# Optimization experiments

Hardware: AMD Instinct MI355X
Metric: run time of the kernel (lower is better)

Reference implementation:

```python
import jax, jax.numpy as jnp
import numpy as np

V = 100000
NNZ = 1600000
B = 4
C_IN = 64
C_HID = 128
C_OUT = 64
K = 4
BN_EPS = 1e-5


def cheb_conv(x, rows, cols, vals, W, b):
    # x: (B, Cin, V); W: (K, Cin, Cout); b: (Cout,)
    Bn, Cin, Vn = x.shape
    Kn = W.shape[0]

    def spmm(y):  # y: (V, F) -> L @ y via edge-list scatter-add
        return jax.ops.segment_sum(vals[:, None] * y[cols], rows, num_segments=Vn)

    x0 = jnp.transpose(x, (2, 0, 1)).reshape(Vn, Bn * Cin)  # (V, B*Cin)
    xs = [x0]
    if Kn > 1:
        x1 = spmm(x0)
        xs.append(x1)
        for _ in range(2, Kn):
            x2 = 2.0 * spmm(x1) - x0  # Chebyshev recurrence
            xs.append(x2)
            x0, x1 = x1, x2
    Xk = jnp.stack(xs, 0).reshape(Kn, Vn, Bn, Cin)  # (K, V, B, Cin)
    out = jnp.einsum('kvbi,kio->bov', Xk, W)  # (B, Cout, V)
    return out + b[None, :, None]


def batch_norm(x, gamma, beta):
    # BatchNorm1d on (B, C, V): stats over (B, V), biased variance (training mode)
    mean = jnp.mean(x, axis=(0, 2), keepdims=True)
    var = jnp.mean(jnp.square(x - mean), axis=(0, 2), keepdims=True)
    xn = (x - mean) * jax.lax.rsqrt(var + BN_EPS)
    return xn * gamma[None, :, None] + beta[None, :, None]


def setup_inputs() -> dict:
    key = jax.random.key(0)
    ks = jax.random.split(key, 8)
    x = jax.random.normal(ks[0], (B, C_IN, V), dtype=jnp.float32)
    lap_rows = jax.random.randint(ks[1], (NNZ,), 0, V, dtype=jnp.int32)
    lap_cols = jax.random.randint(ks[2], (NNZ,), 0, V, dtype=jnp.int32)
    # scale so the effective Laplacian spectral norm is ~O(1) (Chebyshev assumes rescaled L)
    lap_vals = jax.random.normal(ks[3], (NNZ,), dtype=jnp.float32) * 0.01
    w1 = jax.random.normal(ks[4], (K, C_IN, C_HID), dtype=jnp.float32) * (1.0 / np.sqrt(K * C_IN))
    b1 = jnp.zeros((C_HID,), dtype=jnp.float32)
    bn_gamma = jnp.ones((C_HID,), dtype=jnp.float32)
    bn_beta = jnp.zeros((C_HID,), dtype=jnp.float32)
    w2 = jax.random.normal(ks[5], (K, C_HID, C_OUT), dtype=jnp.float32) * (1.0 / np.sqrt(K * C_HID))
    b2 = jnp.zeros((C_OUT,), dtype=jnp.float32)
    return {"x": x, "lap_rows": lap_rows, "lap_cols": lap_cols, "lap_vals": lap_vals,
            "w1": w1, "b1": b1, "bn_gamma": bn_gamma, "bn_beta": bn_beta,
            "w2": w2, "b2": b2}


def reference(x, lap_rows, lap_cols, lap_vals, w1, b1, bn_gamma, bn_beta, w2, b2):
    out = cheb_conv(x, lap_rows, lap_cols, lap_vals, w1, b1)
    out = jax.nn.relu(out)
    out = batch_norm(out, bn_gamma, bn_beta)
    out = cheb_conv(out, lap_rows, lap_cols, lap_vals, w2, b2)
    # in_channels == out_channels -> resizer is Identity
    return jax.nn.relu(out + x)
```

## Files before the change

kernel.cpp:

```cpp
#include <hip/hip_runtime.h>

#define V 100000
#define NNZ 1600000
#define RSLOT 64

typedef unsigned short ushort_t;
typedef unsigned int uint_t;
typedef unsigned long long ull_t;
typedef __attribute__((ext_vector_type(4))) float f32x4;
typedef __attribute__((ext_vector_type(8))) short bf16x8;

__device__ __forceinline__ float bf2f(ushort_t u) {
    union { uint_t i; float f; } x; x.i = ((uint_t)u) << 16; return x.f;
}
__device__ __forceinline__ ushort_t f2bf(float f) {
    union { float f; uint_t i; } x; x.f = f;
    uint_t u = x.i;
    return (ushort_t)((u + 0x7fffu + ((u >> 16) & 1u)) >> 16);
}
__device__ __forceinline__ float blo(uint_t u) {
    union { uint_t i; float f; } x; x.i = u << 16; return x.f;
}
__device__ __forceinline__ float bhi(uint_t u) {
    union { uint_t i; float f; } x; x.i = u & 0xffff0000u; return x.f;
}
__device__ __forceinline__ uint_t pk(float a, float b) {
    return (uint_t)f2bf(a) | ((uint_t)f2bf(b) << 16);
}
__device__ __forceinline__ void unpack8(uint4 u, float* f) {
    f[0] = blo(u.x); f[1] = bhi(u.x); f[2] = blo(u.y); f[3] = bhi(u.y);
    f[4] = blo(u.z); f[5] = bhi(u.z); f[6] = blo(u.w); f[7] = bhi(u.w);
}
__device__ __forceinline__ uint4 pack8(const float* f) {
    uint4 u;
    u.x = pk(f[0], f[1]); u.y = pk(f[2], f[3]);
    u.z = pk(f[4], f[5]); u.w = pk(f[6], f[7]);
    return u;
}

__global__ void diag_k(float* __restrict__ out, float code) {
    if (threadIdx.x == 0 && blockIdx.x == 0) out[0] = code;
}

__global__ __launch_bounds__(256) void pack_x0_k(const float* __restrict__ x,
                                                 ushort_t* __restrict__ x0) {
    __shared__ float tile[32][33];
    int v0 = blockIdx.x * 32, j0 = blockIdx.y * 32;
    int tx = threadIdx.x & 31, ty = threadIdx.x >> 5;
    for (int jj = ty; jj < 32; jj += 8)
        tile[jj][tx] = x[(size_t)(j0 + jj) * V + v0 + tx];
    __syncthreads();
    for (int vv = ty; vv < 32; vv += 8)
        x0[(size_t)(v0 + vv) * 256 + j0 + tx] = f2bf(tile[tx][vv]);
}

__global__ __launch_bounds__(256) void prep_w_k(const float* __restrict__ w1,
                                                const float* __restrict__ w2,
                                                ushort_t* __restrict__ wp1,
                                                ushort_t* __restrict__ wp2) {
    int idx = blockIdx.x * 256 + threadIdx.x;
    if (idx < 32768) {
        int f = idx;
        int j = f & 7, ch = (f >> 3) & 127, q = (f >> 10) & 3, kb = (f >> 12) & 3, L = (f >> 14) & 1;
        int k = kb * 32 + q * 8 + j;
        int t = L * 2 + (k >> 6), i = k & 63;
        wp1[idx] = f2bf(w1[((size_t)t * 64 + i) * 128 + ch]);
    } else {
        int f = idx - 32768;
        int j = f & 7, o = (f >> 3) & 63, q = (f >> 9) & 3, kb = (f >> 11) & 3, t = (f >> 13) & 3;
        int k = kb * 32 + q * 8 + j;
        wp2[f] = f2bf(w2[((size_t)t * 128 + k) * 64 + o]);
    }
}

__global__ __launch_bounds__(256) void scatter_k(const int* __restrict__ rows,
                                                 const int* __restrict__ cols,
                                                 const float* __restrict__ vals,
                                                 int* __restrict__ cnt,
                                                 int2* __restrict__ edges) {
    int e = blockIdx.x * 256 + threadIdx.x;
    int r = rows[e];
    int pos = atomicAdd(&cnt[r], 1);
    edges[r * RSLOT + pos] = make_int2(cols[e], __float_as_int(vals[e]));
}

__global__ __launch_bounds__(256) void spmm_wave(const int* __restrict__ cnt,
                                                 const int2* __restrict__ edges,
                                                 const ushort_t* __restrict__ y,
                                                 const ushort_t* __restrict__ z,
                                                 float alpha, float beta,
                                                 ushort_t* __restrict__ out) {
    int v = __builtin_amdgcn_readfirstlane((blockIdx.x * 256 + threadIdx.x) >> 6);
    if (v >= V) return;
    int l = threadIdx.x & 63;
    const ushort_t* yl = y + l * 4;

    float a0 = 0.f, a1 = 0.f, a2 = 0.f, a3 = 0.f;
    int e0 = v * RSLOT;
    int e1 = e0 + __builtin_amdgcn_readfirstlane(cnt[v]);
    int e = e0;
    for (; e + 8 <= e1; e += 8) {
        int2 ed[8];
#pragma unroll
        for (int i = 0; i < 8; ++i) ed[i] = edges[e + i];
        uint2 u[8];
#pragma unroll
        for (int i = 0; i < 8; ++i) u[i] = *(const uint2*)(yl + (size_t)ed[i].x * 256);
#pragma unroll
        for (int i = 0; i < 8; ++i) {
            float wv = __int_as_float(ed[i].y);
            a0 += wv * blo(u[i].x);
            a1 += wv * bhi(u[i].x);
            a2 += wv * blo(u[i].y);
            a3 += wv * bhi(u[i].y);
        }
    }
    auto masked4 = [&](int base, int c4) {
        int2 ed[4];
#pragma unroll
        for (int i = 0; i < 4; ++i) ed[i] = edges[i < c4 ? base + i : e0];
        uint2 u[4];
#pragma unroll
        for (int i = 0; i < 4; ++i) u[i] = *(const uint2*)(yl + (size_t)ed[i].x * 256);
#pragma unroll
        for (int i = 0; i < 4; ++i) {
            float wv = (i < c4) ? __int_as_float(ed[i].y) : 0.f;
            a0 += wv * blo(u[i].x);
            a1 += wv * bhi(u[i].x);
            a2 += wv * blo(u[i].y);
            a3 += wv * bhi(u[i].y);
        }
    };
    int rem = e1 - e;
    if (rem > 0) masked4(e, rem > 4 ? 4 : rem);
    if (rem > 4) masked4(e + 4, rem - 4);

    float r0 = alpha * a0, r1 = alpha * a1, r2 = alpha * a2, r3 = alpha * a3;
    if (z) {
        ull_t zt = __builtin_nontemporal_load(
            (const ull_t*)(z + (size_t)v * 256 + l * 4));
        r0 += beta * blo((uint_t)zt);
        r1 += beta * bhi((uint_t)zt);
        r2 += beta * blo((uint_t)(zt >> 32));
        r3 += beta * bhi((uint_t)(zt >> 32));
    }
    uint2 st;
    st.x = (uint_t)f2bf(r0) | ((uint_t)f2bf(r1) << 16);
    st.y = (uint_t)f2bf(r2) | ((uint_t)f2bf(r3) << 16);
    *(uint2*)(out + (size_t)v * 256 + l * 4) = st;
}

__global__ __launch_bounds__(256) void gemm1_mfma(const ushort_t* __restrict__ t0,
                                                  const ushort_t* __restrict__ t1,
                                                  const ushort_t* __restrict__ wp,
                                                  const float* __restrict__ b1,
                                                  ushort_t* __restrict__ rb,
                                                  int first, int last) {
    __shared__ uint4 s_buf[1088];
    uint4* s_a = s_buf;
    float* smem = (float*)s_buf;
    int tid = threadIdx.x;
    int l = tid & 63, w = tid >> 6;
    int q = l >> 4, n16 = l & 15;
    int b = blockIdx.y;
    int v0 = blockIdx.x * 64;

    {
        int row = tid >> 3, c = tid & 7;
        int row2 = row + 32;
        int va = v0 + row;  va = va < V ? va : V - 1;
        int vb = v0 + row2; vb = vb < V ? vb : V - 1;
        size_t ga = (size_t)va * 256 + b * 64 + c * 8;
        size_t gb = (size_t)vb * 256 + b * 64 + c * 8;
        s_a[row * 8 + (c ^ (row & 7))] = *(const uint4*)(t0 + ga);
        s_a[row2 * 8 + (c ^ (row2 & 7))] = *(const uint4*)(t0 + gb);
        s_a[512 + row * 8 + (c ^ (row & 7))] = *(const uint4*)(t1 + ga);
        s_a[512 + row2 * 8 + (c ^ (row2 & 7))] = *(const uint4*)(t1 + gb);
    }
    __syncthreads();

    f32x4 acc[8];
#pragma unroll
    for (int ct = 0; ct < 8; ++ct) acc[ct] = (f32x4){0.f, 0.f, 0.f, 0.f};

    int arow = w * 16 + n16;
#pragma unroll
    for (int kb = 0; kb < 4; ++kb) {
        int T = kb >> 1;
        bf16x8 a = *(const bf16x8*)&s_a[T * 512 + arow * 8 + (((kb & 1) * 4 + q) ^ (arow & 7))];
#pragma unroll
        for (int ct = 0; ct < 8; ++ct) {
            bf16x8 bf = *(const bf16x8*)(wp + (size_t)(((kb * 4 + q) * 128) + ct * 16 + n16) * 8);
            acc[ct] = __builtin_amdgcn_mfma_f32_16x16x32_bf16(a, bf, acc[ct], 0, 0, 0);
        }
    }
    __syncthreads();

    int row_d = tid >> 3;
    int c8 = tid & 7;
#pragma unroll
    for (int h = 0; h < 2; ++h) {
        if (h) __syncthreads();
#pragma unroll
        for (int ct = 0; ct < 4; ++ct)
#pragma unroll
            for (int r = 0; r < 4; ++r)
                smem[(w * 16 + q * 4 + r) * 66 + ct * 16 + n16] = acc[h * 4 + ct][r];
        __syncthreads();

        int ch0 = h * 64 + c8 * 8;
        float bc[8];
        if (last) {
#pragma unroll
            for (int j = 0; j < 8; ++j) bc[j] = b1[ch0 + j];
        }
#pragma unroll
        for (int k = 0; k < 2; ++k) {
            int row = row_d + k * 32;
            int v = v0 + row;
            bool valid = v < V;
            float vals[8];
#pragma unroll
            for (int j = 0; j < 8; ++j) vals[j] = smem[row * 66 + c8 * 8 + j];
            ushort_t* p = rb + (size_t)(valid ? v : 0) * 512 + b * 128 + ch0;
            if (!first && valid) {
                uint4 old = *(const uint4*)p;
                float of[8];
                unpack8(old, of);
#pragma unroll
                for (int j = 0; j < 8; ++j) vals[j] += of[j];
            }
            if (last) {
#pragma unroll
                for (int j = 0; j < 8; ++j) vals[j] = fmaxf(vals[j] + bc[j], 0.f);
            }
            if (valid) *(uint4*)p = pack8(vals);
        }
    }
}

__global__ __launch_bounds__(256) void stats_k(const ushort_t* __restrict__ rb,
                                               float* __restrict__ stats) {
    __shared__ float s_sum[128], s_sq[128];
    int tid = threadIdx.x;
    if (tid < 128) { s_sum[tid] = 0.f; s_sq[tid] = 0.f; }
    __syncthreads();
    int g = tid & 15, t16 = tid >> 4;
    float cs[8], cq[8];
#pragma unroll
    for (int j = 0; j < 8; ++j) { cs[j] = 0.f; cq[j] = 0.f; }
    for (int idx = blockIdx.x * 16 + t16; idx < V * 4; idx += 256 * 16) {
        int v = idx >> 2, bb = idx & 3;
        uint4 u = *(const uint4*)(rb + (size_t)v * 512 + bb * 128 + g * 8);
        float f[8];
        unpack8(u, f);
#pragma unroll
        for (int j = 0; j < 8; ++j) { cs[j] += f[j]; cq[j] += f[j] * f[j]; }
    }
#pragma unroll
    for (int j = 0; j < 8; ++j) {
        cs[j] += __shfl_xor(cs[j], 16); cs[j] += __shfl_xor(cs[j], 32);
        cq[j] += __shfl_xor(cq[j], 16); cq[j] += __shfl_xor(cq[j], 32);
    }
    if ((tid & 63) < 16) {
#pragma unroll
        for (int j = 0; j < 8; ++j) {
            atomicAdd(&s_sum[g * 8 + j], cs[j]);
            atomicAdd(&s_sq[g * 8 + j], cq[j]);
        }
    }
    __syncthreads();
    if (tid < 128) {
        atomicAdd(&stats[tid], s_sum[tid]);
        atomicAdd(&stats[128 + tid], s_sq[tid]);
    }
}

__global__ void finalize_k(const float* __restrict__ stats,
                           const float* __restrict__ gamma,
                           const float* __restrict__ beta,
                           float* __restrict__ ss) {
    int c = threadIdx.x;
    float n = (float)(4 * V);
    float mean = stats[c] / n;
    float var = stats[128 + c] / n - mean * mean;
    float inv = rsqrtf(var + 1e-5f);
    float sc = gamma[c] * inv;
    ss[c] = sc;
    ss[128 + c] = beta[c] - mean * sc;
}

__global__ __launch_bounds__(256) void gemmC_mfma(const ushort_t* __restrict__ rb,
                                                  const ushort_t* __restrict__ wp,
                                                  const ushort_t* S,
                                                  const float* __restrict__ ss,
                                                  ushort_t* P) {
    __shared__ float s_ss[256];
    __shared__ uint4 s_buf[1088];
    uint4* s_rb = s_buf;
    float* smem = (float*)s_buf;
    int tid = threadIdx.x;
    s_ss[tid] = ss[tid];
    int l = tid & 63, w = tid >> 6;
    int q = l >> 4, n16 = l & 15;
    int b = blockIdx.y;
    int v0 = blockIdx.x * 64;

#pragma unroll
    for (int k = 0; k < 4; ++k) {
        int idx = tid + k * 256;
        int row = idx >> 4, c = idx & 15;
        int v = v0 + row; v = v < V ? v : V - 1;
        s_rb[row * 16 + (c ^ (row & 7))] = *(const uint4*)(rb + (size_t)v * 512 + b * 128 + c * 8);
    }
    __syncthreads();

    f32x4 acc[4];
#pragma unroll
    for (int ct = 0; ct < 4; ++ct) acc[ct] = (f32x4){0.f, 0.f, 0.f, 0.f};

    int arow = w * 16 + n16;
#pragma unroll
    for (int kb = 0; kb < 4; ++kb) {
        int chl = kb * 32 + q * 8;
        bf16x8 a = *(const bf16x8*)&s_rb[arow * 16 + ((kb * 4 + q) ^ (arow & 7))];
#pragma unroll
        for (int j = 0; j < 8; ++j) {
            float f = bf2f((ushort_t)a[j]) * s_ss[chl + j] + s_ss[128 + chl + j];
            a[j] = (short)f2bf(f);
        }
#pragma unroll
        for (int ct = 0; ct < 4; ++ct) {
            bf16x8 bf = *(const bf16x8*)(wp + (size_t)(((kb * 4 + q) * 64) + ct * 16 + n16) * 8);
            acc[ct] = __builtin_amdgcn_mfma_f32_16x16x32_bf16(a, bf, acc[ct], 0, 0, 0);
        }
    }
    __syncthreads();

#pragma unroll
    for (int ct = 0; ct < 4; ++ct)
#pragma unroll
        for (int r = 0; r < 4; ++r)
            smem[(w * 16 + q * 4 + r) * 66 + ct * 16 + n16] = acc[ct][r];
    __syncthreads();

#pragma unroll
    for (int k = 0; k < 2; ++k) {
        int seg = tid + k * 256;
        int row = seg >> 3;
        int o0 = (seg & 7) * 8;
        int v = v0 + row;
        if (v >= V) continue;
        float vals[8];
#pragma unroll
        for (int j = 0; j < 8; ++j) vals[j] = smem[row * 66 + o0 + j];
        size_t idx = (size_t)v * 256 + b * 64 + o0;
        if (S) {
            uint4 sv = *(const uint4*)(S + idx);
            float sf[8];
            unpack8(sv, sf);
#pragma unroll
            for (int j = 0; j < 8; ++j) vals[j] += sf[j];
        }
        *(uint4*)(P + idx) = pack8(vals);
    }
}

__global__ __launch_bounds__(256) void gemm2_final(const ushort_t* __restrict__ rb,
                                                   const ushort_t* __restrict__ wp,
                                                   const ushort_t* __restrict__ Tb,
                                                   const float* __restrict__ b2,
                                                   const float* __restrict__ xres,
                                                   const float* __restrict__ ss,
                                                   float* __restrict__ out) {
    __shared__ float s_ss[256];
    __shared__ float s_b2[64];
    __shared__ uint_t s_tb[64 * 36];
    __shared__ uint4 s_rb[1024];
    int tid = threadIdx.x;
    s_ss[tid] = ss[tid];
    if (tid < 64) s_b2[tid] = b2[tid];
    int l = tid & 63, w = tid >> 6;
    int q = l >> 4, n16 = l & 15;
    int b = blockIdx.y;
    int v0 = blockIdx.x * 64;

#pragma unroll
    for (int k = 0; k < 2; ++k) {
        int seg = tid + k * 256;
        int row = seg >> 3, c = seg & 7;
        uint4 t = make_uint4(0u, 0u, 0u, 0u);
        if (v0 + row < V) t = *(const uint4*)(Tb + (size_t)(v0 + row) * 256 + b * 64 + c * 8);
        *(uint4*)&s_tb[row * 36 + c * 4] = t;
    }
#pragma unroll
    for (int k = 0; k < 4; ++k) {
        int idx = tid + k * 256;
        int row = idx >> 4, c = idx & 15;
        int v = v0 + row; v = v < V ? v : V - 1;
        s_rb[row * 16 + (c ^ (row & 7))] = *(const uint4*)(rb + (size_t)v * 512 + b * 128 + c * 8);
    }
    __syncthreads();

    f32x4 acc[4];
#pragma unroll
    for (int rt = 0; rt < 4; ++rt) acc[rt] = (f32x4){0.f, 0.f, 0.f, 0.f};

    int vl = w * 16 + n16;
#pragma unroll
    for (int kb = 0; kb < 4; ++kb) {
        int chl = kb * 32 + q * 8;
        bf16x8 t = *(const bf16x8*)&s_rb[vl * 16 + ((kb * 4 + q) ^ (vl & 7))];
#pragma unroll
        for (int j = 0; j < 8; ++j) {
            float f = bf2f((ushort_t)t[j]) * s_ss[chl + j] + s_ss[128 + chl + j];
            t[j] = (short)f2bf(f);
        }
#pragma unroll
        for (int rt = 0; rt < 4; ++rt) {
            bf16x8 af = *(const bf16x8*)(wp + (size_t)(((kb * 4 + q) * 64) + rt * 16 + n16) * 8);
            acc[rt] = __builtin_amdgcn_mfma_f32_16x16x32_bf16(af, t, acc[rt], 0, 0, 0);
        }
    }

    int v = v0 + vl;
    bool valid = v < V;
    int vv = valid ? v : 0;
#pragma unroll
    for (int rt = 0; rt < 4; ++rt)
#pragma unroll
        for (int r = 0; r < 4; ++r) {
            int o = rt * 16 + q * 4 + r;
            uint_t pr = s_tb[vl * 36 + rt * 8 + q * 2 + (r >> 1)];
            float tb = (r & 1) ? bhi(pr) : blo(pr);
            size_t idx = (size_t)(b * 64 + o) * V + vv;
            float val = acc[rt][r] + tb + s_b2[o] + xres[idx];
            if (valid) out[idx] = fmaxf(val, 0.f);
        }
}

extern "C" void kernel_launch(void* const* d_in, const int* in_sizes, int n_in,
                              void* d_out, int out_size, void* d_ws, size_t ws_size,
                              hipStream_t stream) {
    const float* x = (const float*)d_in[0];
    const int* lap_rows = (const int*)d_in[1];
    const int* lap_cols = (const int*)d_in[2];
    const float* lap_vals = (const float*)d_in[3];
    const float* w1 = (const float*)d_in[4];
    const float* b1 = (const float*)d_in[5];
    const float* bn_gamma = (const float*)d_in[6];
    const float* bn_beta = (const float*)d_in[7];
    const float* w2 = (const float*)d_in[8];
    const float* b2 = (const float*)d_in[9];
    float* out = (float*)d_out;

    char* ws = (char*)d_ws;
    size_t off = 0;
    auto alloc = [&](size_t bytes) {
        size_t r = off;
        off = (off + bytes + 255) & ~(size_t)255;
        return r;
    };
    size_t reg1_off = alloc((size_t)V * 512 * 2);
    size_t rb_off   = alloc((size_t)V * 512 * 2);
    size_t ed_off   = alloc((size_t)V * RSLOT * 8);
    size_t cur_off  = alloc((size_t)V * 4);
    size_t st_off   = alloc(256 * 4);
    size_t ss_off   = alloc(256 * 4);
    size_t wp1_off  = alloc(32768 * 2);
    size_t wp2_off  = alloc(32768 * 2);

    if (ws_size < off) {
        diag_k<<<1, 64, 0, stream>>>(out, 1000.f + (float)(ws_size >> 20));
        return;
    }

    ushort_t* slotA = (ushort_t*)(ws + reg1_off);
    ushort_t* slotB = slotA + (size_t)V * 256;
    ushort_t* rb = (ushort_t*)(ws + rb_off);
    int2* edges = (int2*)(ws + ed_off);
    int* cnt = (int*)(ws + cur_off);
    float* stats = (float*)(ws + st_off);
    float* ss = (float*)(ws + ss_off);
    ushort_t* wp1 = (ushort_t*)(ws + wp1_off);
    ushort_t* wp2 = (ushort_t*)(ws + wp2_off);

    const int SG = (V + 3) / 4;
    const ushort_t* nullu = (const ushort_t*)nullptr;

    hipMemsetAsync(cnt, 0, (size_t)V * 4, stream);
    hipMemsetAsync(stats, 0, 256 * 4, stream);

    pack_x0_k<<<dim3(V / 32, 8), 256, 0, stream>>>(x, slotA);
    prep_w_k<<<256, 256, 0, stream>>>(w1, w2, wp1, wp2);
    scatter_k<<<NNZ / 256, 256, 0, stream>>>(lap_rows, lap_cols, lap_vals, cnt, edges);

    dim3 g1((V + 63) / 64, 4);

    spmm_wave<<<SG, 256, 0, stream>>>(cnt, edges, slotA, nullu, 1.f, 0.f, slotB);
    gemm1_mfma<<<g1, 256, 0, stream>>>(slotA, slotB, wp1, b1, rb, 1, 0);
    spmm_wave<<<SG, 256, 0, stream>>>(cnt, edges, slotB, slotA, 2.f, -1.f, slotA);
    spmm_wave<<<SG, 256, 0, stream>>>(cnt, edges, slotA, slotB, 2.f, -1.f, slotB);
    gemm1_mfma<<<g1, 256, 0, stream>>>(slotA, slotB, wp1 + 16384, b1, rb, 0, 1);

    stats_k<<<256, 256, 0, stream>>>(rb, stats);
    finalize_k<<<1, 128, 0, stream>>>(stats, bn_gamma, bn_beta, ss);

    gemmC_mfma<<<g1, 256, 0, stream>>>(rb, wp2 + 3 * 8192, nullu, ss, slotA);
    spmm_wave<<<SG, 256, 0, stream>>>(cnt, edges, slotA, nullu, 2.f, 0.f, slotB);
    gemmC_mfma<<<g1, 256, 0, stream>>>(rb, wp2 + 2 * 8192, slotB, ss, slotB);
    spmm_wave<<<SG, 256, 0, stream>>>(cnt, edges, slotB, slotA, 2.f, -1.f, slotA);
    gemmC_mfma<<<g1, 256, 0, stream>>>(rb, wp2 + 1 * 8192, slotA, ss, slotA);
    spmm_wave<<<SG, 256, 0, stream>>>(cnt, edges, slotA, slotB, 1.f, -1.f, slotB);
    gemm2_final<<<g1, 256, 0, stream>>>(rb, wp2, slotB, b2, x, ss, out);
}
```

Before: 1.330 ms.

## Fuse BN statistics into layer-1 GEMM and merge K=4 GEMM passes

Folds the batch-norm sum and sum-of-squares reduction into the epilogue of the first-layer GEMM, so the separate stats kernel no longer re-reads the hidden activation buffer. When workspace allows, it also keeps all four Chebyshev terms in separate buffers and runs a single GEMM over K=256. This avoids the read-modify-write of the partial result and saves one launch. The cost is a larger workspace, which falls back to the old two-pass GEMM path if unavailable, plus extra shuffles and atomics in the epilogue.

New measurement: 1.410 ms. +6.0%, slower.

```diff
diff --git a/kernel.cpp b/kernel.cpp
--- a/kernel.cpp
+++ b/kernel.cpp
@@ -155,8 +155,10 @@
                                                   const ushort_t* __restrict__ wp,
                                                   const float* __restrict__ b1,
                                                   ushort_t* __restrict__ rb,
+                                                  float* __restrict__ stats,
                                                   int first, int last) {
     __shared__ uint4 s_buf[1088];
+    __shared__ float s_sum[128], s_sq[128];
     uint4* s_a = s_buf;
     float* smem = (float*)s_buf;
     int tid = threadIdx.x;
@@ -164,6 +166,7 @@
     int q = l >> 4, n16 = l & 15;
     int b = blockIdx.y;
     int v0 = blockIdx.x * 64;
+    if (tid < 128) { s_sum[tid] = 0.f; s_sq[tid] = 0.f; }
 
     {
         int row = tid >> 3, c = tid & 7;
@@ -214,6 +217,9 @@
 #pragma unroll
             for (int j = 0; j < 8; ++j) bc[j] = b1[ch0 + j];
         }
+        float csum[8], csq[8];
+#pragma unroll
+        for (int j = 0; j < 8; ++j) { csum[j] = 0.f; csq[j] = 0.f; }
 #pragma unroll
         for (int k = 0; k < 2; ++k) {
             int row = row_d + k * 32;
@@ -233,40 +239,145 @@
             if (last) {
 #pragma unroll
                 for (int j = 0; j < 8; ++j) vals[j] = fmaxf(vals[j] + bc[j], 0.f);
+                if (valid) {
+#pragma unroll
+                    for (int j = 0; j < 8; ++j) { csum[j] += vals[j]; csq[j] += vals[j] * vals[j]; }
+                }
             }
             if (valid) *(uint4*)p = pack8(vals);
         }
-    }
-}
-
-__global__ __launch_bounds__(256) void stats_k(const ushort_t* __restrict__ rb,
-                                               float* __restrict__ stats) {
+        if (last) {
+#pragma unroll
+            for (int j = 0; j < 8; ++j) {
+                csum[j] += __shfl_xor(csum[j], 8);
+                csum[j] += __shfl_xor(csum[j], 16);
+                csum[j] += __shfl_xor(csum[j], 32);
+                csq[j] += __shfl_xor(csq[j], 8);
+                csq[j] += __shfl_xor(csq[j], 16);
+                csq[j] += __shfl_xor(csq[j], 32);
+            }
+            if (l == c8) {
+#pragma unroll
+                for (int j = 0; j < 8; ++j) {
+                    atomicAdd(&s_sum[ch0 + j], csum[j]);
+                    atomicAdd(&s_sq[ch0 + j], csq[j]);
+                }
+            }
+        }
+    }
+    if (last) {
+        __syncthreads();
+        if (tid < 128) {
+            atomicAdd(&stats[tid], s_sum[tid]);
+            atomicAdd(&stats[128 + tid], s_sq[tid]);
+        }
+    }
+}
+
+__global__ __launch_bounds__(256) void gemm1K256(const ushort_t* __restrict__ x0b,
+                                                 const ushort_t* __restrict__ x1b,
+                                                 const ushort_t* __restrict__ x2b,
+                                                 const ushort_t* __restrict__ x3b,
+                                                 const ushort_t* __restrict__ wp,
+                                                 const float* __restrict__ b1,
+                                                 ushort_t* __restrict__ rb,
+                                                 float* __restrict__ stats) {
+    __shared__ uint4 s_buf[1088];
     __shared__ float s_sum[128], s_sq[128];
+    uint4* s_a = s_buf;
+    float* smem = (float*)s_buf;
     int tid = threadIdx.x;
+    int l = tid & 63, w = tid >> 6;
+    int q = l >> 4, n16 = l & 15;
+    int b = blockIdx.y;
+    int v0 = blockIdx.x * 64;
     if (tid < 128) { s_sum[tid] = 0.f; s_sq[tid] = 0.f; }
-    __syncthreads();
-    int g = tid & 15, t16 = tid >> 4;
-    float cs[8], cq[8];
-#pragma unroll
-    for (int j = 0; j < 8; ++j) { cs[j] = 0.f; cq[j] = 0.f; }
-    for (int idx = blockIdx.x * 16 + t16; idx < V * 4; idx += 256 * 16) {
-        int v = idx >> 2, bb = idx & 3;
-        uint4 u = *(const uint4*)(rb + (size_t)v * 512 + bb * 128 + g * 8);
-        float f[8];
-        unpack8(u, f);
-#pragma unroll
-        for (int j = 0; j < 8; ++j) { cs[j] += f[j]; cq[j] += f[j] * f[j]; }
-    }
-#pragma unroll
-    for (int j = 0; j < 8; ++j) {
-        cs[j] += __shfl_xor(cs[j], 16); cs[j] += __shfl_xor(cs[j], 32);
-        cq[j] += __shfl_xor(cq[j], 16); cq[j] += __shfl_xor(cq[j], 32);
-    }
-    if ((tid & 63) < 16) {
+
+    f32x4 acc[8];
+#pragma unroll
+    for (int ct = 0; ct < 8; ++ct) acc[ct] = (f32x4){0.f, 0.f, 0.f, 0.f};
+
+    int arow = w * 16 + n16;
+    int srow = tid >> 3, sc = tid & 7;
+    int srow2 = srow + 32;
+    int va = v0 + srow;  va = va < V ? va : V - 1;
+    int vb = v0 + srow2; vb = vb < V ? vb : V - 1;
+    int sw1 = sc ^ (srow & 7), sw2 = sc ^ (srow2 & 7);
+    size_t ga = (size_t)va * 256 + b * 64 + sc * 8;
+    size_t gb = (size_t)vb * 256 + b * 64 + sc * 8;
+
+#pragma unroll
+    for (int p = 0; p < 2; ++p) {
+        if (p) __syncthreads();
+        const ushort_t* t0 = p ? x2b : x0b;
+        const ushort_t* t1 = p ? x3b : x1b;
+        s_a[srow * 8 + sw1] = *(const uint4*)(t0 + ga);
+        s_a[srow2 * 8 + sw2] = *(const uint4*)(t0 + gb);
+        s_a[512 + srow * 8 + sw1] = *(const uint4*)(t1 + ga);
+        s_a[512 + srow2 * 8 + sw2] = *(const uint4*)(t1 + gb);
+        __syncthreads();
+#pragma unroll
+        for (int kb = 0; kb < 4; ++kb) {
+            int T = kb >> 1;
+            bf16x8 a = *(const bf16x8*)&s_a[T * 512 + arow * 8 +
+                                            ((((kb & 1) * 4) + q) ^ (arow & 7))];
+#pragma unroll
+            for (int ct = 0; ct < 8; ++ct) {
+                bf16x8 bf = *(const bf16x8*)(wp + (size_t)(((p * 16 + kb * 4 + q) * 128) + ct * 16 + n16) * 8);
+                acc[ct] = __builtin_amdgcn_mfma_f32_16x16x32_bf16(a, bf, acc[ct], 0, 0, 0);
+            }
+        }
+    }
+    __syncthreads();
+
+    int row_d = tid >> 3, c8 = tid & 7;
+#pragma unroll
+    for (int h = 0; h < 2; ++h) {
+        if (h) __syncthreads();
+#pragma unroll
+        for (int ct = 0; ct < 4; ++ct)
+#pragma unroll
+            for (int r = 0; r < 4; ++r)
+                smem[(w * 16 + q * 4 + r) * 66 + ct * 16 + n16] = acc[h * 4 + ct][r];
+        __syncthreads();
+
+        int ch0 = h * 64 + c8 * 8;
+        float bc[8];
+#pragma unroll
+        for (int j = 0; j < 8; ++j) bc[j] = b1[ch0 + j];
+        float csum[8], csq[8];
+#pragma unroll
+        for (int j = 0; j < 8; ++j) { csum[j] = 0.f; csq[j] = 0.f; }
+#pragma unroll
+        for (int k = 0; k < 2; ++k) {
+            int row = row_d + k * 32;
+            int v = v0 + row;
+            bool valid = v < V;
+            float vals[8];
+#pragma unroll
+            for (int j = 0; j < 8; ++j)
+                vals[j] = fmaxf(smem[row * 66 + c8 * 8 + j] + bc[j], 0.f);
+            if (valid) {
+#pragma unroll
+                for (int j = 0; j < 8; ++j) { csum[j] += vals[j]; csq[j] += vals[j] * vals[j]; }
+                *(uint4*)(rb + (size_t)v * 512 + b * 128 + ch0) = pack8(vals);
+            }
+        }
 #pragma unroll
         for (int j = 0; j < 8; ++j) {
-            atomicAdd(&s_sum[g * 8 + j], cs[j]);
-            atomicAdd(&s_sq[g * 8 + j], cq[j]);
+            csum[j] += __shfl_xor(csum[j], 8);
+            csum[j] += __shfl_xor(csum[j], 16);
+            csum[j] += __shfl_xor(csum[j], 32);
+            csq[j] += __shfl_xor(csq[j], 8);
+            csq[j] += __shfl_xor(csq[j], 16);
+            csq[j] += __shfl_xor(csq[j], 32);
+        }
+        if (l == c8) {
+#pragma unroll
+            for (int j = 0; j < 8; ++j) {
+                atomicAdd(&s_sum[ch0 + j], csum[j]);
+                atomicAdd(&s_sq[ch0 + j], csq[j]);
+            }
         }
     }
     __syncthreads();
@@ -469,11 +580,15 @@
     size_t ss_off   = alloc(256 * 4);
     size_t wp1_off  = alloc(32768 * 2);
     size_t wp2_off  = alloc(32768 * 2);
-
-    if (ws_size < off) {
+    size_t need_small = off;
+    size_t scd_off  = alloc((size_t)V * 512 * 2);
+    size_t need_big = off;
+
+    if (ws_size < need_small) {
         diag_k<<<1, 64, 0, stream>>>(out, 1000.f + (float)(ws_size >> 20));
         return;
     }
+    bool big = ws_size >= need_big;
 
     ushort_t* slotA = (ushort_t*)(ws + reg1_off);
     ushort_t* slotB = slotA + (size_t)V * 256;
@@ -484,6 +599,8 @@
     float* ss = (float*)(ws + ss_off);
     ushort_t* wp1 = (ushort_t*)(ws + wp1_off);
     ushort_t* wp2 = (ushort_t*)(ws + wp2_off);
+    ushort_t* slotC = (ushort_t*)(ws + scd_off);
+    ushort_t* slotD = slotC + (size_t)V * 256;
 
     const int SG = (V + 3) / 4;
     const ushort_t* nullu = (const ushort_t*)nullptr;
@@ -497,13 +614,19 @@
 
     dim3 g1((V + 63) / 64, 4);
 
-    spmm_wave<<<SG, 256, 0, stream>>>(cnt, edges, slotA, nullu, 1.f, 0.f, slotB);
-    gemm1_mfma<<<g1, 256, 0, stream>>>(slotA, slotB, wp1, b1, rb, 1, 0);
-    spmm_wave<<<SG, 256, 0, stream>>>(cnt, edges, slotB, slotA, 2.f, -1.f, slotA);
-    spmm_wave<<<SG, 256, 0, stream>>>(cnt, edges, slotA, slotB, 2.f, -1.f, slotB);
-    gemm1_mfma<<<g1, 256, 0, stream>>>(slotA, slotB, wp1 + 16384, b1, rb, 0, 1);
-
-    stats_k<<<256, 256, 0, stream>>>(rb, stats);
+    if (big) {
+        spmm_wave<<<SG, 256, 0, stream>>>(cnt, edges, slotA, nullu, 1.f, 0.f, slotB);
+        spmm_wave<<<SG, 256, 0, stream>>>(cnt, edges, slotB, slotA, 2.f, -1.f, slotC);
+        spmm_wave<<<SG, 256, 0, stream>>>(cnt, edges, slotC, slotB, 2.f, -1.f, slotD);
+        gemm1K256<<<g1, 256, 0, stream>>>(slotA, slotB, slotC, slotD, wp1, b1, rb, stats);
+    } else {
+        spmm_wave<<<SG, 256, 0, stream>>>(cnt, edges, slotA, nullu, 1.f, 0.f, slotB);
+        gemm1_mfma<<<g1, 256, 0, stream>>>(slotA, slotB, wp1, b1, rb, stats, 1, 0);
+        spmm_wave<<<SG, 256, 0, stream>>>(cnt, edges, slotB, slotA, 2.f, -1.f, slotA);
+        spmm_wave<<<SG, 256, 0, stream>>>(cnt, edges, slotA, slotB, 2.f, -1.f, slotB);
+        gemm1_mfma<<<g1, 256, 0, stream>>>(slotA, slotB, wp1 + 16384, b1, rb, stats, 0, 1);
+    }
+
     finalize_k<<<1, 128, 0, stream>>>(stats, bn_gamma, bn_beta, ss);
 
     gemmC_mfma<<<g1, 256, 0, stream>>>(rb, wp2 + 3 * 8192, nullu, ss, slotA);
```
